# Performance work log

Measured on AMD Instinct MI355X. Metric: run time of the kernel, lower is better.

The kernel has to match this reference:

```python
import jax, jax.numpy as jnp
import numpy as np

B, D, C, K = 131072, 512, 5, 10  # batch, emb_dim, num_classes, k experts


def setup_inputs() -> dict:
    key = jax.random.key(0)
    k1, k2, k3, k4, k5 = jax.random.split(key, 5)
    s = 1.0 / np.sqrt(D)
    return {
        "emb": jax.random.normal(k1, (B, D), dtype=jnp.float32),
        "We": jax.random.normal(k2, (K, D, C), dtype=jnp.float32) * s,
        "be": jax.random.normal(k3, (K, C), dtype=jnp.float32) * s,
        "Wg": jax.random.normal(k4, (D, K), dtype=jnp.float32) * s,
        "bg": jax.random.normal(k5, (K,), dtype=jnp.float32) * s,
    }


def reference(emb, We, be, Wg, bg):
    # gate: softmax over experts, [B, K]
    g = jax.nn.softmax(emb @ Wg + bg, axis=1)
    # all experts as one batched GEMM: [B, K, C], then ReLU
    e = jax.nn.relu(jnp.einsum('bd,kdc->bkc', emb, We) + be[None, :, :])
    # gate-weighted sum over experts -> [B, C]
    return jnp.einsum('bkc,bk->bc', e, g)
```

## Files before the change

### kernel.cpp

```cpp
#include <hip/hip_runtime.h>
#include <hip/hip_bf16.h>
#include <math.h>

#define BATCH   131072
#define DIM     512
#define NCLS    5
#define NEXP    10
#define NW      60
#define NCOL    64
#define PACK_TPB 256
#define TPB     512
#define ROWS_PER_BLOCK 128
#define EPS_STRIDE 68

typedef short bf16x8 __attribute__((ext_vector_type(8)));
typedef float f32x4  __attribute__((ext_vector_type(4)));

__global__ void pack_w_kernel(const float* __restrict__ We,
                              const float* __restrict__ be,
                              const float* __restrict__ Wg,
                              const float* __restrict__ bg,
                              unsigned short* __restrict__ wfrag,
                              float* __restrict__ bpack) {
    int idx = blockIdx.x * PACK_TPB + threadIdx.x;
    int c    = idx >> 11;
    int t    = (idx >> 9) & 3;
    int lane = (idx >> 3) & 63;
    int j    = idx & 7;
    int d = c * 32 + (lane >> 4) * 8 + j;
    int n = t * 16 + (lane & 15);
    float v = 0.0f;
    if (n < NEXP) {
        v = Wg[d * NEXP + n];
    } else if (n < NW) {
        int k  = (n - NEXP) / NCLS;
        int cc = (n - NEXP) % NCLS;
        v = We[(k * DIM + d) * NCLS + cc];
    }
    wfrag[idx] = __builtin_bit_cast(unsigned short, __float2bfloat16(v));
    if (idx < NCOL) {
        float bv = 0.0f;
        if (idx < NEXP) bv = bg[idx];
        else if (idx < NW) {
            int k  = (idx - NEXP) / NCLS;
            int cc = (idx - NEXP) % NCLS;
            bv = be[k * NCLS + cc];
        }
        bpack[idx] = bv;
    }
}

__global__ __launch_bounds__(TPB) void moe_mfma_kernel(
        const float* __restrict__ emb,
        const float4* __restrict__ wfrag4,
        const float* __restrict__ bpack,
        float* __restrict__ out) {
    __shared__ float4 smem4[4096];

    const int tid = threadIdx.x;

    #pragma unroll
    for (int i = 0; i < 8; ++i)
        smem4[i * TPB + tid] = wfrag4[i * TPB + tid];
    __syncthreads();

    const int w = tid >> 6;
    const int L = tid & 63;
    const int r = L & 15;
    const int q = L >> 4;

    const size_t rowBase = (size_t)blockIdx.x * ROWS_PER_BLOCK + w * 16;
    const float* arow = emb + (rowBase + r) * DIM + q * 8;
    const bf16x8* bl = reinterpret_cast<const bf16x8*>(smem4);

    f32x4 acc0 = {0.f, 0.f, 0.f, 0.f};
    f32x4 acc1 = acc0, acc2 = acc0, acc3 = acc0;

    #pragma unroll 4
    for (int c = 0; c < DIM / 32; ++c) {
        const float4* a4 = reinterpret_cast<const float4*>(arow + (size_t)c * 32);
        float4 a0 = a4[0];
        float4 a1 = a4[1];
        bf16x8 b0 = bl[(c * 4 + 0) * 64 + L];
        bf16x8 b1 = bl[(c * 4 + 1) * 64 + L];
        bf16x8 b2 = bl[(c * 4 + 2) * 64 + L];
        bf16x8 b3 = bl[(c * 4 + 3) * 64 + L];
        float av[8] = {a0.x, a0.y, a0.z, a0.w, a1.x, a1.y, a1.z, a1.w};
        bf16x8 af;
        #pragma unroll
        for (int j = 0; j < 8; ++j)
            af[j] = (short)__builtin_bit_cast(unsigned short, __float2bfloat16(av[j]));
        acc0 = __builtin_amdgcn_mfma_f32_16x16x32_bf16(af, b0, acc0, 0, 0, 0);
        acc1 = __builtin_amdgcn_mfma_f32_16x16x32_bf16(af, b1, acc1, 0, 0, 0);
        acc2 = __builtin_amdgcn_mfma_f32_16x16x32_bf16(af, b2, acc2, 0, 0, 0);
        acc3 = __builtin_amdgcn_mfma_f32_16x16x32_bf16(af, b3, acc3, 0, 0, 0);
    }

    __syncthreads();
    float* eps = reinterpret_cast<float*>(smem4);
    #pragma unroll
    for (int i = 0; i < 4; ++i) {
        int rowl = w * 16 + q * 4 + i;
        eps[rowl * EPS_STRIDE +  0 + r] = acc0[i];
        eps[rowl * EPS_STRIDE + 16 + r] = acc1[i];
        eps[rowl * EPS_STRIDE + 32 + r] = acc2[i];
        eps[rowl * EPS_STRIDE + 48 + r] = acc3[i];
    }
    __syncthreads();

    if (tid < ROWS_PER_BLOCK) {
        const float* row = eps + tid * EPS_STRIDE;
        float g[NEXP];
        float m = -INFINITY;
        #pragma unroll
        for (int k = 0; k < NEXP; ++k) {
            g[k] = row[k] + bpack[k];
            m = fmaxf(m, g[k]);
        }
        float s = 0.0f;
        #pragma unroll
        for (int k = 0; k < NEXP; ++k) {
            g[k] = __expf(g[k] - m);
            s += g[k];
        }
        float inv = 1.0f / s;

        float o[NCLS] = {0.f, 0.f, 0.f, 0.f, 0.f};
        #pragma unroll
        for (int k = 0; k < NEXP; ++k) {
            float gk = g[k] * inv;
            #pragma unroll
            for (int cc = 0; cc < NCLS; ++cc) {
                int n = NEXP + k * NCLS + cc;
                float e = row[n] + bpack[n];
                e = fmaxf(e, 0.0f);
                o[cc] = fmaf(gk, e, o[cc]);
            }
        }
        size_t ob = ((size_t)blockIdx.x * ROWS_PER_BLOCK + tid) * NCLS;
        #pragma unroll
        for (int cc = 0; cc < NCLS; ++cc) out[ob + cc] = o[cc];
    }
}

extern "C" void kernel_launch(void* const* d_in, const int* in_sizes, int n_in,
                              void* d_out, int out_size, void* d_ws, size_t ws_size,
                              hipStream_t stream) {
    const float* emb = (const float*)d_in[0];
    const float* We  = (const float*)d_in[1];
    const float* be  = (const float*)d_in[2];
    const float* Wg  = (const float*)d_in[3];
    const float* bg  = (const float*)d_in[4];
    float* out = (float*)d_out;

    unsigned short* wfrag = (unsigned short*)d_ws;
    float* bpack = (float*)((char*)d_ws + 32768 * sizeof(unsigned short));

    pack_w_kernel<<<(16 * 4 * 64 * 8) / PACK_TPB, PACK_TPB, 0, stream>>>(
        We, be, Wg, bg, wfrag, bpack);
    moe_mfma_kernel<<<BATCH / ROWS_PER_BLOCK, TPB, 0, stream>>>(
        emb, (const float4*)wfrag, bpack, out);
}
```

Baseline: 362.0 us.

## Process 32 rows per wave with register double-buffered emb prefetch

Each wave now computes two 16-row MFMA tiles, 32 rows in total, so every B fragment read from LDS is reused twice, and each block handles 256 rows. The emb loads are software-pipelined two chunks ahead in registers, and the main loop is fully unrolled so more global loads are in flight. The eps staging buffer is resized with an odd stride of 65 to avoid bank conflicts. In exchange, register pressure is higher and there are half as many blocks, which may reduce occupancy for this memory-bound streaming kernel.

```diff
diff --git a/kernel.cpp b/kernel.cpp
--- a/kernel.cpp
+++ b/kernel.cpp
@@ -10,8 +10,10 @@
 #define NCOL    64
 #define PACK_TPB 256
 #define TPB     512
-#define ROWS_PER_BLOCK 128
-#define EPS_STRIDE 68
+#define ROWS_PER_WAVE 32
+#define ROWS_PER_BLOCK 256
+#define NCHUNK  16
+#define EPS_STRIDE 65
 
 typedef short bf16x8 __attribute__((ext_vector_type(8)));
 typedef float f32x4  __attribute__((ext_vector_type(4)));
@@ -50,12 +52,25 @@
     }
 }
 
+static __device__ __forceinline__ bf16x8 cvt8(float4 x, float4 y) {
+    bf16x8 o;
+    o[0] = (short)__builtin_bit_cast(unsigned short, __float2bfloat16(x.x));
+    o[1] = (short)__builtin_bit_cast(unsigned short, __float2bfloat16(x.y));
+    o[2] = (short)__builtin_bit_cast(unsigned short, __float2bfloat16(x.z));
+    o[3] = (short)__builtin_bit_cast(unsigned short, __float2bfloat16(x.w));
+    o[4] = (short)__builtin_bit_cast(unsigned short, __float2bfloat16(y.x));
+    o[5] = (short)__builtin_bit_cast(unsigned short, __float2bfloat16(y.y));
+    o[6] = (short)__builtin_bit_cast(unsigned short, __float2bfloat16(y.z));
+    o[7] = (short)__builtin_bit_cast(unsigned short, __float2bfloat16(y.w));
+    return o;
+}
+
 __global__ __launch_bounds__(TPB) void moe_mfma_kernel(
         const float* __restrict__ emb,
         const float4* __restrict__ wfrag4,
         const float* __restrict__ bpack,
         float* __restrict__ out) {
-    __shared__ float4 smem4[4096];
+    __shared__ float4 smem4[4160];
 
     const int tid = threadIdx.x;
 
@@ -69,42 +84,64 @@
     const int r = L & 15;
     const int q = L >> 4;
 
-    const size_t rowBase = (size_t)blockIdx.x * ROWS_PER_BLOCK + w * 16;
-    const float* arow = emb + (rowBase + r) * DIM + q * 8;
+    const size_t wrb = (size_t)blockIdx.x * ROWS_PER_BLOCK + w * ROWS_PER_WAVE;
+    const float* a0p = emb + (wrb + r) * DIM + q * 8;
+    const float* a1p = a0p + 16 * DIM;
     const bf16x8* bl = reinterpret_cast<const bf16x8*>(smem4);
 
-    f32x4 acc0 = {0.f, 0.f, 0.f, 0.f};
-    f32x4 acc1 = acc0, acc2 = acc0, acc3 = acc0;
-
-    #pragma unroll 4
-    for (int c = 0; c < DIM / 32; ++c) {
-        const float4* a4 = reinterpret_cast<const float4*>(arow + (size_t)c * 32);
-        float4 a0 = a4[0];
-        float4 a1 = a4[1];
+    f32x4 acc[2][4];
+    #pragma unroll
+    for (int t2 = 0; t2 < 2; ++t2)
+        #pragma unroll
+        for (int ct = 0; ct < 4; ++ct)
+            acc[t2][ct] = (f32x4){0.f, 0.f, 0.f, 0.f};
+
+    float4 pa[2][4];
+    #pragma unroll
+    for (int s = 0; s < 2; ++s) {
+        pa[s][0] = *reinterpret_cast<const float4*>(a0p + s * 32);
+        pa[s][1] = *reinterpret_cast<const float4*>(a0p + s * 32 + 4);
+        pa[s][2] = *reinterpret_cast<const float4*>(a1p + s * 32);
+        pa[s][3] = *reinterpret_cast<const float4*>(a1p + s * 32 + 4);
+    }
+
+    #pragma unroll
+    for (int c = 0; c < NCHUNK; ++c) {
+        const int s = c & 1;
+        bf16x8 af0 = cvt8(pa[s][0], pa[s][1]);
+        bf16x8 af1 = cvt8(pa[s][2], pa[s][3]);
+        if (c < NCHUNK - 2) {
+            pa[s][0] = *reinterpret_cast<const float4*>(a0p + (c + 2) * 32);
+            pa[s][1] = *reinterpret_cast<const float4*>(a0p + (c + 2) * 32 + 4);
+            pa[s][2] = *reinterpret_cast<const float4*>(a1p + (c + 2) * 32);
+            pa[s][3] = *reinterpret_cast<const float4*>(a1p + (c + 2) * 32 + 4);
+        }
         bf16x8 b0 = bl[(c * 4 + 0) * 64 + L];
         bf16x8 b1 = bl[(c * 4 + 1) * 64 + L];
         bf16x8 b2 = bl[(c * 4 + 2) * 64 + L];
         bf16x8 b3 = bl[(c * 4 + 3) * 64 + L];
-        float av[8] = {a0.x, a0.y, a0.z, a0.w, a1.x, a1.y, a1.z, a1.w};
-        bf16x8 af;
-        #pragma unroll
-        for (int j = 0; j < 8; ++j)
-            af[j] = (short)__builtin_bit_cast(unsigned short, __float2bfloat16(av[j]));
-        acc0 = __builtin_amdgcn_mfma_f32_16x16x32_bf16(af, b0, acc0, 0, 0, 0);
-        acc1 = __builtin_amdgcn_mfma_f32_16x16x32_bf16(af, b1, acc1, 0, 0, 0);
-        acc2 = __builtin_amdgcn_mfma_f32_16x16x32_bf16(af, b2, acc2, 0, 0, 0);
-        acc3 = __builtin_amdgcn_mfma_f32_16x16x32_bf16(af, b3, acc3, 0, 0, 0);
+        acc[0][0] = __builtin_amdgcn_mfma_f32_16x16x32_bf16(af0, b0, acc[0][0], 0, 0, 0);
+        acc[0][1] = __builtin_amdgcn_mfma_f32_16x16x32_bf16(af0, b1, acc[0][1], 0, 0, 0);
+        acc[0][2] = __builtin_amdgcn_mfma_f32_16x16x32_bf16(af0, b2, acc[0][2], 0, 0, 0);
+        acc[0][3] = __builtin_amdgcn_mfma_f32_16x16x32_bf16(af0, b3, acc[0][3], 0, 0, 0);
+        acc[1][0] = __builtin_amdgcn_mfma_f32_16x16x32_bf16(af1, b0, acc[1][0], 0, 0, 0);
+        acc[1][1] = __builtin_amdgcn_mfma_f32_16x16x32_bf16(af1, b1, acc[1][1], 0, 0, 0);
+        acc[1][2] = __builtin_amdgcn_mfma_f32_16x16x32_bf16(af1, b2, acc[1][2], 0, 0, 0);
+        acc[1][3] = __builtin_amdgcn_mfma_f32_16x16x32_bf16(af1, b3, acc[1][3], 0, 0, 0);
     }
 
     __syncthreads();
     float* eps = reinterpret_cast<float*>(smem4);
     #pragma unroll
-    for (int i = 0; i < 4; ++i) {
-        int rowl = w * 16 + q * 4 + i;
-        eps[rowl * EPS_STRIDE +  0 + r] = acc0[i];
-        eps[rowl * EPS_STRIDE + 16 + r] = acc1[i];
-        eps[rowl * EPS_STRIDE + 32 + r] = acc2[i];
-        eps[rowl * EPS_STRIDE + 48 + r] = acc3[i];
+    for (int t2 = 0; t2 < 2; ++t2) {
+        #pragma unroll
+        for (int i = 0; i < 4; ++i) {
+            int rowl = w * ROWS_PER_WAVE + t2 * 16 + q * 4 + i;
+            eps[rowl * EPS_STRIDE +  0 + r] = acc[t2][0][i];
+            eps[rowl * EPS_STRIDE + 16 + r] = acc[t2][1][i];
+            eps[rowl * EPS_STRIDE + 32 + r] = acc[t2][2][i];
+            eps[rowl * EPS_STRIDE + 48 + r] = acc[t2][3][i];
+        }
     }
     __syncthreads();
 
```

Result: slower. 372.3 us (+2.8%).

## Stage emb rows in LDS as swizzled bf16 with coalesced loads; read weights from global

Applied to the files above, without the earlier changes.

The activation tile is now loaded cooperatively with fully coalesced float4 reads, converted to bf16 and written into a swizzled LDS layout. The MFMA loop reads A fragments from LDS, while the packed weight fragments are read straight from global/L2 instead of being staged in LDS. Blocks shrink to 128 threads handling 32 rows with launch bounds allowing two blocks per CU. The aim is to fix the strided per-lane global loads of the old version, at the cost of more blocks and repeated weight reads from cache.

```diff
diff --git a/kernel.cpp b/kernel.cpp
--- a/kernel.cpp
+++ b/kernel.cpp
@@ -9,12 +9,18 @@
 #define NW      60
 #define NCOL    64
 #define PACK_TPB 256
-#define TPB     512
-#define ROWS_PER_BLOCK 128
-#define EPS_STRIDE 68
+#define TPB     128
+#define BLOCK_ROWS 32
+#define NCHUNK  16
+#define EPS_STRIDE 65
 
 typedef short bf16x8 __attribute__((ext_vector_type(8)));
 typedef float f32x4  __attribute__((ext_vector_type(4)));
+
+static __device__ __forceinline__ unsigned short bfb(float f) {
+    __hip_bfloat16 h = __float2bfloat16(f);
+    return __builtin_bit_cast(unsigned short, h);
+}
 
 __global__ void pack_w_kernel(const float* __restrict__ We,
                               const float* __restrict__ be,
@@ -37,7 +43,7 @@
         int cc = (n - NEXP) % NCLS;
         v = We[(k * DIM + d) * NCLS + cc];
     }
-    wfrag[idx] = __builtin_bit_cast(unsigned short, __float2bfloat16(v));
+    wfrag[idx] = bfb(v);
     if (idx < NCOL) {
         float bv = 0.0f;
         if (idx < NEXP) bv = bg[idx];
@@ -50,46 +56,59 @@
     }
 }
 
-__global__ __launch_bounds__(TPB) void moe_mfma_kernel(
+__global__ __launch_bounds__(TPB, 2) void moe_mfma_kernel(
         const float* __restrict__ emb,
         const float4* __restrict__ wfrag4,
         const float* __restrict__ bpack,
         float* __restrict__ out) {
-    __shared__ float4 smem4[4096];
+    __shared__ uint2 ldsA[4096];
 
     const int tid = threadIdx.x;
+    const int w   = tid >> 6;
+    const int L   = tid & 63;
+
+    const float4* embv = reinterpret_cast<const float4*>(emb);
+    const size_t base4 = (size_t)blockIdx.x * (BLOCK_ROWS * DIM / 4);
+    const int c_t     = tid >> 3;
+    const int colpart = (c_t << 6) + (((tid >> 1) & 3) << 4);
+    const int key     = c_t & 7;
+    const int jh      = tid & 1;
 
     #pragma unroll
-    for (int i = 0; i < 8; ++i)
-        smem4[i * TPB + tid] = wfrag4[i * TPB + tid];
+    for (int batch = 0; batch < 4; ++batch) {
+        float4 v[8];
+        #pragma unroll
+        for (int i = 0; i < 8; ++i) {
+            int p = batch * 8 + i;
+            v[i] = embv[base4 + (size_t)p * (DIM / 4) + tid];
+        }
+        #pragma unroll
+        for (int i = 0; i < 8; ++i) {
+            int p = batch * 8 + i;
+            int g = p >> 4, r = p & 15;
+            int slot = (g << 10) + colpart + r;
+            int phys = slot ^ key;
+            uint2 pk;
+            pk.x = (unsigned)bfb(v[i].x) | ((unsigned)bfb(v[i].y) << 16);
+            pk.y = (unsigned)bfb(v[i].z) | ((unsigned)bfb(v[i].w) << 16);
+            ldsA[phys * 2 + jh] = pk;
+        }
+    }
     __syncthreads();
 
-    const int w = tid >> 6;
-    const int L = tid & 63;
-    const int r = L & 15;
-    const int q = L >> 4;
-
-    const size_t rowBase = (size_t)blockIdx.x * ROWS_PER_BLOCK + w * 16;
-    const float* arow = emb + (rowBase + r) * DIM + q * 8;
-    const bf16x8* bl = reinterpret_cast<const bf16x8*>(smem4);
+    const bf16x8* ap = reinterpret_cast<const bf16x8*>(ldsA);
+    const bf16x8* bp = reinterpret_cast<const bf16x8*>(wfrag4);
 
     f32x4 acc0 = {0.f, 0.f, 0.f, 0.f};
     f32x4 acc1 = acc0, acc2 = acc0, acc3 = acc0;
 
     #pragma unroll 4
-    for (int c = 0; c < DIM / 32; ++c) {
-        const float4* a4 = reinterpret_cast<const float4*>(arow + (size_t)c * 32);
-        float4 a0 = a4[0];
-        float4 a1 = a4[1];
-        bf16x8 b0 = bl[(c * 4 + 0) * 64 + L];
-        bf16x8 b1 = bl[(c * 4 + 1) * 64 + L];
-        bf16x8 b2 = bl[(c * 4 + 2) * 64 + L];
-        bf16x8 b3 = bl[(c * 4 + 3) * 64 + L];
-        float av[8] = {a0.x, a0.y, a0.z, a0.w, a1.x, a1.y, a1.z, a1.w};
-        bf16x8 af;
-        #pragma unroll
-        for (int j = 0; j < 8; ++j)
-            af[j] = (short)__builtin_bit_cast(unsigned short, __float2bfloat16(av[j]));
+    for (int c = 0; c < NCHUNK; ++c) {
+        bf16x8 af = ap[((w * 16 + c) << 6) + (L ^ (c & 7))];
+        bf16x8 b0 = bp[((c * 4 + 0) << 6) + L];
+        bf16x8 b1 = bp[((c * 4 + 1) << 6) + L];
+        bf16x8 b2 = bp[((c * 4 + 2) << 6) + L];
+        bf16x8 b3 = bp[((c * 4 + 3) << 6) + L];
         acc0 = __builtin_amdgcn_mfma_f32_16x16x32_bf16(af, b0, acc0, 0, 0, 0);
         acc1 = __builtin_amdgcn_mfma_f32_16x16x32_bf16(af, b1, acc1, 0, 0, 0);
         acc2 = __builtin_amdgcn_mfma_f32_16x16x32_bf16(af, b2, acc2, 0, 0, 0);
@@ -97,7 +116,9 @@
     }
 
     __syncthreads();
-    float* eps = reinterpret_cast<float*>(smem4);
+    float* eps = reinterpret_cast<float*>(ldsA);
+    const int r = L & 15;
+    const int q = L >> 4;
     #pragma unroll
     for (int i = 0; i < 4; ++i) {
         int rowl = w * 16 + q * 4 + i;
@@ -108,7 +129,7 @@
     }
     __syncthreads();
 
-    if (tid < ROWS_PER_BLOCK) {
+    if (tid < BLOCK_ROWS) {
         const float* row = eps + tid * EPS_STRIDE;
         float g[NEXP];
         float m = -INFINITY;
@@ -137,7 +158,7 @@
                 o[cc] = fmaf(gk, e, o[cc]);
             }
         }
-        size_t ob = ((size_t)blockIdx.x * ROWS_PER_BLOCK + tid) * NCLS;
+        size_t ob = ((size_t)blockIdx.x * BLOCK_ROWS + tid) * NCLS;
         #pragma unroll
         for (int cc = 0; cc < NCLS; ++cc) out[ob + cc] = o[cc];
     }
@@ -158,6 +179,6 @@
 
     pack_w_kernel<<<(16 * 4 * 64 * 8) / PACK_TPB, PACK_TPB, 0, stream>>>(
         We, be, Wg, bg, wfrag, bpack);
-    moe_mfma_kernel<<<BATCH / ROWS_PER_BLOCK, TPB, 0, stream>>>(
+    moe_mfma_kernel<<<BATCH / BLOCK_ROWS, TPB, 0, stream>>>(
         emb, (const float4*)wfrag, bpack, out);
 }
```

After: 385.0 us. 6.4% more time.
